# Optimization experiments

Hardware: AMD Instinct MI355X
Metric: run time of the kernel (lower is better)

Reference implementation:

```python
import jax, jax.numpy as jnp
import numpy as np
import math

INPUT_FRAMES = 12
FUTURE_FRAMES = 26
T_STEPS = INPUT_FRAMES + FUTURE_FRAMES - 1  # 37
HD = 64   # hidden_dim
D = 16    # d_attn
CIN = 3   # input channels (time='stable')
COUT = 2  # output_dim
H, W = 24, 48


def conv2d(x, w, b, pad):
    # x: (N,C,H,W), w: (O,I,kh,kw)
    y = jax.lax.conv_general_dilated(x, w, (1, 1), [(pad, pad), (pad, pad)],
                                     dimension_numbers=('NCHW', 'OIHW', 'NCHW'))
    return y + b[None, :, None, None]


def spatial_attn(q, k, v):
    # q,k,v: (N,C,S); attention over spatial dim S
    scale = 1.0 / math.sqrt(q.shape[1])
    scores = jnp.einsum('ncs,nct->nst', q, k) * scale  # (N,S,S)
    a = jax.nn.softmax(scores, axis=-1)
    return jnp.einsum('nst,nct->ncs', a, v)


def setup_inputs() -> dict:
    key = jax.random.key(0)
    ks = jax.random.split(key, 8)
    s = 0.05
    inp = {
        'input_x': jax.random.normal(ks[0], (16, T_STEPS, H, W, CIN), dtype=jnp.float32),
        # ConvLSTM gate conv: in = CIN+HD, out = 4*HD, 3x3
        'conv_w': jax.random.normal(ks[1], (4 * HD, CIN + HD, 3, 3), dtype=jnp.float32) * s,
        'conv_b': jnp.zeros((4 * HD,), jnp.float32),
        # SA memory module
        'h_w': jax.random.normal(ks[2], (3 * D, HD, 1, 1), dtype=jnp.float32) * s,
        'h_b': jnp.zeros((3 * D,), jnp.float32),
        'm_w': jax.random.normal(ks[3], (2 * D, HD, 1, 1), dtype=jnp.float32) * s,
        'm_b': jnp.zeros((2 * D,), jnp.float32),
        'z_w': jax.random.normal(ks[4], (D, 2 * D, 1, 1), dtype=jnp.float32) * s,
        'z_b': jnp.zeros((D,), jnp.float32),
        'o_w': jax.random.normal(ks[5], (3 * HD, HD + D, 3, 3), dtype=jnp.float32) * s,
        'o_b': jnp.zeros((3 * HD,), jnp.float32),
        # final 1x1 projection to output_dim
        'out_w': jax.random.normal(ks[6], (COUT, HD, 1, 1), dtype=jnp.float32) * s,
        'out_b': jnp.zeros((COUT,), jnp.float32),
    }
    return inp


def reference(input_x, conv_w, conv_b, h_w, h_b, m_w, m_b, z_w, z_b, o_w, o_b, out_w, out_b):
    x = jnp.transpose(input_x, (0, 1, 4, 2, 3))  # (N,T,C,H,W)
    N = x.shape[0]
    S = H * W

    h0 = jnp.zeros((N, HD, H, W), x.dtype)
    carry0 = (h0, h0, h0, jnp.zeros((N, COUT, H, W), x.dtype))

    def step(carry, inp_t):
        h, c, m, prev_out = carry
        xt, t = inp_t  # xt: (N,CIN,H,W), t: scalar
        autoreg = jnp.concatenate([prev_out, xt[:, 2:]], axis=1)
        feed = jnp.where(t < INPUT_FRAMES, xt, autoreg)
        # ConvLSTM gates
        comb = conv2d(jnp.concatenate([feed, h], axis=1), conv_w, conv_b, 1)
        ci, cf, co, cg = jnp.split(comb, 4, axis=1)
        i = jax.nn.sigmoid(ci)
        f = jax.nn.sigmoid(cf)
        o = jax.nn.sigmoid(co)
        g = jnp.tanh(cg)
        c = f * c + i * g
        h = o * jnp.tanh(c)
        # self-attention memory
        hq, hk, hv = jnp.split(conv2d(h, h_w, h_b, 0), 3, axis=1)
        mk, mv = jnp.split(conv2d(m, m_w, m_b, 0), 2, axis=1)
        Zh = spatial_attn(hq.reshape(N, D, S), hk.reshape(N, D, S), hv.reshape(N, D, S))
        Zm = spatial_attn(hq.reshape(N, D, S), mk.reshape(N, D, S), mv.reshape(N, D, S))
        Z = conv2d(jnp.concatenate([Zh.reshape(N, D, H, W), Zm.reshape(N, D, H, W)], axis=1), z_w, z_b, 0)
        iog = conv2d(jnp.concatenate([Z, h], axis=1), o_w, o_b, 1)
        si, sg, so = jnp.split(iog, 3, axis=1)
        si = jax.nn.sigmoid(si)
        sg = jnp.tanh(sg)
        m = si * sg + (1.0 - si) * m
        h = jax.nn.sigmoid(so) * m
        out = conv2d(h, out_w, out_b, 0)
        return (h, c, m, out), out

    xs = (jnp.transpose(x, (1, 0, 2, 3, 4)), jnp.arange(T_STEPS))
    _, outs = jax.lax.scan(step, carry0, xs)
    outputs = jnp.transpose(outs, (1, 0, 2, 3, 4))  # (N,T,COUT,H,W)

    nino = outputs[:, -FUTURE_FRAMES:, 0, 10:13, 19:30].mean(axis=(2, 3))  # (N,26)
    nino_pred = (nino[:, :-2] + nino[:, 1:-1] + nino[:, 2:]) / 3.0          # (N,24)
    return outputs, nino_pred
```

## Files before the change

kernel.cpp:

```cpp
#include <hip/hip_runtime.h>
#include <math.h>

#define HD 64
#define DATT 16
#define NCIN 3
#define NCOUT 2
#define HH 24
#define WW 48
#define SS (HH*WW)
#define NB 16
#define TSTEPS 37
#define INPUT_FRAMES 12

#define PR 26
#define PC 52
#define PHW (PR*PC)

#define OFF_H     0
#define OFF_C     1384448
#define OFF_M     2564096
#define OFF_FEED  3743744
#define OFF_Z     3808640
#define ZERO_END  4154752
#define OFF_QKV   4154752
#define OFF_MKV   5039488
#define OFF_HB    5629312
#define OFF_IOG   8873344
#define OFF_BF2   12412288
#define OFF_BF    12596864

typedef __attribute__((ext_vector_type(8))) short short8;
typedef __attribute__((ext_vector_type(4))) float f32x4;

__device__ __forceinline__ float sigmoidf_(float x) {
    return 1.0f / (1.0f + __expf(-x));
}
__device__ __forceinline__ unsigned short f2bf(float f) {
    unsigned u = __float_as_uint(f);
    unsigned r = (u + 0x7fffu + ((u >> 16) & 1u)) >> 16;
    return (unsigned short)r;
}
__device__ __forceinline__ float bf2f(unsigned short b) {
    return __uint_as_float(((unsigned)b) << 16);
}
__device__ __forceinline__ unsigned packbf(float f) {
    unsigned short hi = f2bf(f);
    unsigned short lo = f2bf(f - bf2f(hi));
    return ((unsigned)lo << 16) | (unsigned)hi;
}
__device__ __forceinline__ float unpackbf(unsigned pk) {
    return __uint_as_float(pk << 16) + __uint_as_float(pk & 0xffff0000u);
}
__device__ __forceinline__ unsigned cvt_pk_bf16(float a, float b) {
    unsigned r;
    asm("v_cvt_pk_bf16_f32 %0, %1, %2" : "=v"(r) : "v"(a), "v"(b));
    return r;
}
__device__ __forceinline__ int permrow(int t) {
    int kb = t >> 5, tl = t & 31;
    int quad = tl >> 3, rr = tl & 7;
    return kb * 32 + ((rr >= 4) ? 16 : 0) + quad * 4 + (rr & 3);
}

__global__ void k_zero(float* __restrict__ p, int n4) {
    int i = blockIdx.x * blockDim.x + threadIdx.x;
    if (i < n4) ((float4*)p)[i] = make_float4(0.f, 0.f, 0.f, 0.f);
}

__global__ void k_prep_bf2(const float* __restrict__ cw, unsigned short* __restrict__ bbuf) {
    int idx = blockIdx.x * 256 + threadIdx.x;
    if (idx >= 344064) return;
    int j    = idx & 7;
    int lane = (idx >> 3) & 63;
    int ki   = (idx >> 9) % 21;
    int nt   = (idx / 10752) % 16;
    int p    = idx / 172032;
    int k = ki * 32 + (lane >> 4) * 8 + j;
    int ncol = nt * 16 + (lane & 15);
    unsigned short v = 0;
    if (k < 648) {
        int c = k % 72, kt = k / 72;
        if (c < 67) {
            float w = cw[ncol * 603 + c * 9 + kt];
            unsigned short hi = f2bf(w);
            v = (p == 0) ? hi : f2bf(w - bf2f(hi));
        }
    }
    bbuf[idx] = v;
}

__global__ void k_prep_bf(const float* __restrict__ ow, unsigned short* __restrict__ bbuf) {
    int idx = blockIdx.x * 256 + threadIdx.x;
    if (idx >= 282624) return;
    int j    = idx & 7;
    int lane = (idx >> 3) & 63;
    int ki   = (idx >> 9) % 23;
    int nt   = (idx / 11776) % 12;
    int p    = idx / 141312;
    int k = ki * 32 + (lane >> 4) * 8 + j;
    int ncol = nt * 16 + (lane & 15);
    unsigned short v = 0;
    if (k < 720) {
        int c = k % 80, kt = k / 80;
        float w = ow[ncol * 720 + c * 9 + kt];
        unsigned short hi = f2bf(w);
        v = (p == 0) ? hi : f2bf(w - bf2f(hi));
    }
    bbuf[idx] = v;
}

__global__ void k_feed0(const float* __restrict__ x, unsigned* __restrict__ feed) {
    int i = blockIdx.x * blockDim.x + threadIdx.x;
    if (i >= NB * 3 * SS) return;
    int s = i % SS;
    int ch = (i / SS) % 3;
    int n = i / (3 * SS);
    int y = s / WW, xx = s % WW;
    float v = x[(((size_t)(n * TSTEPS + 0) * HH + y) * WW + xx) * NCIN + ch];
    feed[((size_t)(n * 3 + ch) * PR + (y + 1)) * PC + (xx + 1)] = packbf(v);
}

#define RSTR2 304
#define ZROW2 (156*RSTR2)
__global__ __launch_bounds__(256) void k_conv_lstm_mfma(
    const unsigned* __restrict__ feed, const unsigned* __restrict__ hin,
    const unsigned short* __restrict__ bbuf, const float* __restrict__ cb,
    float* __restrict__ c, unsigned* __restrict__ hout)
{
    __shared__ __align__(16) int lds[156 * 76 + 76 + 8];
    const int n  = blockIdx.x;
    const int nb = blockIdx.y;
    const int y0 = blockIdx.z;
    const int tid = threadIdx.x;

    const unsigned* fbase = feed + (size_t)n * 3 * PHW;
    const unsigned* hbase = hin + (size_t)n * HD * PHW;
    for (int e = tid; e < 1404; e += 256) {
        int grp = e / 156;
        int r2  = e - grp * 156;
        int pr = r2 / 52, pc = r2 - pr * 52;
        int cc0 = grp * 8;
        unsigned v[8];
#pragma unroll
        for (int j = 0; j < 8; ++j) {
            int cc = cc0 + j;
            unsigned t = 0;
            if (cc < 3)        t = fbase[(size_t)cc * PHW + (y0 + pr) * PC + pc];
            else if (cc < 67)  t = hbase[(size_t)(cc - 3) * PHW + (y0 + pr) * PC + pc];
            v[j] = t;
        }
        union { unsigned u[4]; short8 s; } hi8, lo8;
#pragma unroll
        for (int p = 0; p < 4; ++p) {
            hi8.u[p] = (v[2 * p] & 0xffffu) | (v[2 * p + 1] << 16);
            lo8.u[p] = (v[2 * p] >> 16) | (v[2 * p + 1] & 0xffff0000u);
        }
        char* rowp = (char*)lds + r2 * RSTR2 + cc0 * 2;
        *(short8*)rowp = hi8.s;
        *(short8*)(rowp + 144) = lo8.s;
    }
    for (int i = tid; i < 76; i += 256) lds[156 * 76 + i] = 0;
    __syncthreads();

    const int wv = tid >> 6;
    const int lane = tid & 63;
    const int mcol = lane & 15;
    const int quad = lane >> 4;

    f32x4 acc[2][3];
#pragma unroll
    for (int jg = 0; jg < 2; ++jg)
#pragma unroll
        for (int xt = 0; xt < 3; ++xt) acc[jg][xt] = (f32x4){0.f, 0.f, 0.f, 0.f};

    const unsigned short* b0 = bbuf + ((size_t)(wv * 4 + nb * 2 + 0) * 21) * 512 + lane * 8;
    const unsigned short* b1 = bbuf + ((size_t)(wv * 4 + nb * 2 + 1) * 21) * 512 + lane * 8;

    short8 cb0h = *(const short8*)(b0);
    short8 cb0l = *(const short8*)(b0 + 172032);
    short8 cb1h = *(const short8*)(b1);
    short8 cb1l = *(const short8*)(b1 + 172032);
    short8 pb0h = *(const short8*)(b0 + 512);
    short8 pb0l = *(const short8*)(b0 + 512 + 172032);
    short8 pb1h = *(const short8*)(b1 + 512);
    short8 pb1l = *(const short8*)(b1 + 512 + 172032);

    const char* lp = (const char*)lds;

    for (int ki = 0; ki < 21; ++ki) {
        int kn = (ki + 2 <= 20) ? (ki + 2) * 512 : 20 * 512;
        short8 qb0h = *(const short8*)(b0 + kn);
        short8 qb0l = *(const short8*)(b0 + kn + 172032);
        short8 qb1h = *(const short8*)(b1 + kn);
        short8 qb1l = *(const short8*)(b1 + kn + 172032);

        int k0 = ki * 32 + quad * 8;
        int abyte, stepb;
        if (k0 < 648) {
            int kt = k0 / 72;
            int c0 = k0 - kt * 72;
            int dy = kt / 3, dx = kt - dy * 3;
            abyte = (dy * 52 + mcol + dx) * RSTR2 + c0 * 2;
            stepb = 16 * RSTR2;
        } else {
            abyte = ZROW2; stepb = 0;
        }
        short8 xh0 = *(const short8*)(lp + abyte);
        short8 xl0 = *(const short8*)(lp + abyte + 144);
        short8 xh1 = *(const short8*)(lp + abyte + stepb);
        short8 xl1 = *(const short8*)(lp + abyte + stepb + 144);
        short8 xh2 = *(const short8*)(lp + abyte + 2 * stepb);
        short8 xl2 = *(const short8*)(lp + abyte + 2 * stepb + 144);

        acc[0][0] = __builtin_amdgcn_mfma_f32_16x16x32_bf16(xh0, cb0h, acc[0][0], 0, 0, 0);
        acc[0][0] = __builtin_amdgcn_mfma_f32_16x16x32_bf16(xh0, cb0l, acc[0][0], 0, 0, 0);
        acc[0][0] = __builtin_amdgcn_mfma_f32_16x16x32_bf16(xl0, cb0h, acc[0][0], 0, 0, 0);
        acc[1][0] = __builtin_amdgcn_mfma_f32_16x16x32_bf16(xh0, cb1h, acc[1][0], 0, 0, 0);
        acc[1][0] = __builtin_amdgcn_mfma_f32_16x16x32_bf16(xh0, cb1l, acc[1][0], 0, 0, 0);
        acc[1][0] = __builtin_amdgcn_mfma_f32_16x16x32_bf16(xl0, cb1h, acc[1][0], 0, 0, 0);
        acc[0][1] = __builtin_amdgcn_mfma_f32_16x16x32_bf16(xh1, cb0h, acc[0][1], 0, 0, 0);
        acc[0][1] = __builtin_amdgcn_mfma_f32_16x16x32_bf16(xh1, cb0l, acc[0][1], 0, 0, 0);
        acc[0][1] = __builtin_amdgcn_mfma_f32_16x16x32_bf16(xl1, cb0h, acc[0][1], 0, 0, 0);
        acc[1][1] = __builtin_amdgcn_mfma_f32_16x16x32_bf16(xh1, cb1h, acc[1][1], 0, 0, 0);
        acc[1][1] = __builtin_amdgcn_mfma_f32_16x16x32_bf16(xh1, cb1l, acc[1][1], 0, 0, 0);
        acc[1][1] = __builtin_amdgcn_mfma_f32_16x16x32_bf16(xl1, cb1h, acc[1][1], 0, 0, 0);
        acc[0][2] = __builtin_amdgcn_mfma_f32_16x16x32_bf16(xh2, cb0h, acc[0][2], 0, 0, 0);
        acc[0][2] = __builtin_amdgcn_mfma_f32_16x16x32_bf16(xh2, cb0l, acc[0][2], 0, 0, 0);
        acc[0][2] = __builtin_amdgcn_mfma_f32_16x16x32_bf16(xl2, cb0h, acc[0][2], 0, 0, 0);
        acc[1][2] = __builtin_amdgcn_mfma_f32_16x16x32_bf16(xh2, cb1h, acc[1][2], 0, 0, 0);
        acc[1][2] = __builtin_amdgcn_mfma_f32_16x16x32_bf16(xh2, cb1l, acc[1][2], 0, 0, 0);
        acc[1][2] = __builtin_amdgcn_mfma_f32_16x16x32_bf16(xl2, cb1h, acc[1][2], 0, 0, 0);

        cb0h = pb0h; cb0l = pb0l; cb1h = pb1h; cb1l = pb1l;
        pb0h = qb0h; pb0l = qb0l; pb1h = qb1h; pb1l = qb1l;
    }

    __syncthreads();
    float* exch = (float*)lds;
#pragma unroll
    for (int jg = 0; jg < 2; ++jg)
#pragma unroll
        for (int xt = 0; xt < 3; ++xt)
#pragma unroll
            for (int r = 0; r < 4; ++r)
                exch[((wv * 2 + jg) * 3 + xt) * 272 + (quad * 4 + r) * 17 + mcol] = acc[jg][xt][r];
    __syncthreads();

    const int ch32 = tid & 31;
    const int xg = tid >> 5;
    const int jg = ch32 >> 4, col = ch32 & 15;
    const int gch = nb * 32 + ch32;
    const float bi = cb[gch], bfv = cb[64 + gch], bo = cb[128 + gch], bg = cb[192 + gch];
    size_t cbase = ((size_t)(n * HD + gch) * HH + y0) * WW;
    unsigned* hp = hout + ((size_t)(n * HD + gch) * PR + y0 + 1) * PC + 1;
#pragma unroll
    for (int k = 0; k < 6; ++k) {
        int x = xg * 6 + k;
        int xt = x >> 4, row = x & 15;
        float iv = sigmoidf_(exch[((0 * 2 + jg) * 3 + xt) * 272 + row * 17 + col] + bi);
        float fv = sigmoidf_(exch[((1 * 2 + jg) * 3 + xt) * 272 + row * 17 + col] + bfv);
        float ov = sigmoidf_(exch[((2 * 2 + jg) * 3 + xt) * 272 + row * 17 + col] + bo);
        float gv = tanhf    (exch[((3 * 2 + jg) * 3 + xt) * 272 + row * 17 + col] + bg);
        float cold = c[cbase + x];
        float cn = fv * cold + iv * gv;
        float hn = ov * tanhf(cn);
        c[cbase + x] = cn;
        hp[x] = packbf(hn);
    }
}

#define RSTR 328
#define ZROW (156*RSTR)
__global__ __launch_bounds__(192) void k_conv_sa(
    const unsigned* __restrict__ Zin, const unsigned* __restrict__ hin,
    const unsigned short* __restrict__ bbuf, const float* __restrict__ ob,
    float* __restrict__ m, unsigned* __restrict__ hout)
{
    __shared__ __align__(16) int lds[156 * 82 + 82 + 8];
    const int n  = blockIdx.x;
    const int cbk = blockIdx.y;
    const int y0 = blockIdx.z;
    const int tid = threadIdx.x;

    const unsigned* zbase = Zin + (size_t)n * DATT * PHW;
    const unsigned* hbase = hin + (size_t)n * HD * PHW;
    for (int e = tid; e < 1560; e += 192) {
        int grp = e / 156;
        int r2  = e - grp * 156;
        int pr = r2 / 52, pc = r2 - pr * 52;
        int cc0 = grp * 8;
        unsigned v[8];
#pragma unroll
        for (int j = 0; j < 8; ++j) {
            int cc = cc0 + j;
            const unsigned* src = (cc < 16) ? (zbase + (size_t)cc * PHW)
                                            : (hbase + (size_t)(cc - 16) * PHW);
            v[j] = src[(y0 + pr) * PC + pc];
        }
        union { unsigned u[4]; short8 s; } hi8, lo8;
#pragma unroll
        for (int p = 0; p < 4; ++p) {
            hi8.u[p] = (v[2 * p] & 0xffffu) | (v[2 * p + 1] << 16);
            lo8.u[p] = (v[2 * p] >> 16) | (v[2 * p + 1] & 0xffff0000u);
        }
        char* rowp = (char*)lds + r2 * RSTR + cc0 * 2;
        *(short8*)rowp = hi8.s;
        *(short8*)(rowp + 160) = lo8.s;
    }
    for (int i = tid; i < 82; i += 192) lds[156 * 82 + i] = 0;
    __syncthreads();

    const int wv = tid >> 6;
    const int lane = tid & 63;
    const int mcol = lane & 15;
    const int quad = lane >> 4;

    f32x4 acc[2][3];
#pragma unroll
    for (int j = 0; j < 2; ++j)
#pragma unroll
        for (int xt = 0; xt < 3; ++xt) acc[j][xt] = (f32x4){0.f, 0.f, 0.f, 0.f};

    const unsigned short* b0 = bbuf + ((size_t)(wv * 4 + cbk * 2 + 0) * 23) * 512 + lane * 8;
    const unsigned short* b1 = bbuf + ((size_t)(wv * 4 + cbk * 2 + 1) * 23) * 512 + lane * 8;

    short8 cb0h = *(const short8*)(b0);
    short8 cb0l = *(const short8*)(b0 + 141312);
    short8 cb1h = *(const short8*)(b1);
    short8 cb1l = *(const short8*)(b1 + 141312);
    short8 pb0h = *(const short8*)(b0 + 512);
    short8 pb0l = *(const short8*)(b0 + 512 + 141312);
    short8 pb1h = *(const short8*)(b1 + 512);
    short8 pb1l = *(const short8*)(b1 + 512 + 141312);

    const char* lp = (const char*)lds;

    for (int ki = 0; ki < 23; ++ki) {
        int kn = (ki + 2 <= 22) ? (ki + 2) * 512 : 22 * 512;
        short8 qb0h = *(const short8*)(b0 + kn);
        short8 qb0l = *(const short8*)(b0 + kn + 141312);
        short8 qb1h = *(const short8*)(b1 + kn);
        short8 qb1l = *(const short8*)(b1 + kn + 141312);

        int k0 = ki * 32 + quad * 8;
        int abyte, stepb;
        if (k0 < 720) {
            int kt = k0 / 80;
            int c0 = k0 - kt * 80;
            int dy = kt / 3, dx = kt - dy * 3;
            abyte = (dy * 52 + mcol + dx) * RSTR + c0 * 2;
            stepb = 16 * RSTR;
        } else {
            abyte = ZROW; stepb = 0;
        }
        short8 xh0 = *(const short8*)(lp + abyte);
        short8 xl0 = *(const short8*)(lp + abyte + 160);
        short8 xh1 = *(const short8*)(lp + abyte + stepb);
        short8 xl1 = *(const short8*)(lp + abyte + stepb + 160);
        short8 xh2 = *(const short8*)(lp + abyte + 2 * stepb);
        short8 xl2 = *(const short8*)(lp + abyte + 2 * stepb + 160);

        acc[0][0] = __builtin_amdgcn_mfma_f32_16x16x32_bf16(xh0, cb0h, acc[0][0], 0, 0, 0);
        acc[0][0] = __builtin_amdgcn_mfma_f32_16x16x32_bf16(xh0, cb0l, acc[0][0], 0, 0, 0);
        acc[0][0] = __builtin_amdgcn_mfma_f32_16x16x32_bf16(xl0, cb0h, acc[0][0], 0, 0, 0);
        acc[1][0] = __builtin_amdgcn_mfma_f32_16x16x32_bf16(xh0, cb1h, acc[1][0], 0, 0, 0);
        acc[1][0] = __builtin_amdgcn_mfma_f32_16x16x32_bf16(xh0, cb1l, acc[1][0], 0, 0, 0);
        acc[1][0] = __builtin_amdgcn_mfma_f32_16x16x32_bf16(xl0, cb1h, acc[1][0], 0, 0, 0);
        acc[0][1] = __builtin_amdgcn_mfma_f32_16x16x32_bf16(xh1, cb0h, acc[0][1], 0, 0, 0);
        acc[0][1] = __builtin_amdgcn_mfma_f32_16x16x32_bf16(xh1, cb0l, acc[0][1], 0, 0, 0);
        acc[0][1] = __builtin_amdgcn_mfma_f32_16x16x32_bf16(xl1, cb0h, acc[0][1], 0, 0, 0);
        acc[1][1] = __builtin_amdgcn_mfma_f32_16x16x32_bf16(xh1, cb1h, acc[1][1], 0, 0, 0);
        acc[1][1] = __builtin_amdgcn_mfma_f32_16x16x32_bf16(xh1, cb1l, acc[1][1], 0, 0, 0);
        acc[1][1] = __builtin_amdgcn_mfma_f32_16x16x32_bf16(xl1, cb1h, acc[1][1], 0, 0, 0);
        acc[0][2] = __builtin_amdgcn_mfma_f32_16x16x32_bf16(xh2, cb0h, acc[0][2], 0, 0, 0);
        acc[0][2] = __builtin_amdgcn_mfma_f32_16x16x32_bf16(xh2, cb0l, acc[0][2], 0, 0, 0);
        acc[0][2] = __builtin_amdgcn_mfma_f32_16x16x32_bf16(xl2, cb0h, acc[0][2], 0, 0, 0);
        acc[1][2] = __builtin_amdgcn_mfma_f32_16x16x32_bf16(xh2, cb1h, acc[1][2], 0, 0, 0);
        acc[1][2] = __builtin_amdgcn_mfma_f32_16x16x32_bf16(xh2, cb1l, acc[1][2], 0, 0, 0);
        acc[1][2] = __builtin_amdgcn_mfma_f32_16x16x32_bf16(xl2, cb1h, acc[1][2], 0, 0, 0);

        cb0h = pb0h; cb0l = pb0l; cb1h = pb1h; cb1l = pb1l;
        pb0h = qb0h; pb0l = qb0l; pb1h = qb1h; pb1l = qb1l;
    }

    __syncthreads();
    float* exch = (float*)lds;
#pragma unroll
    for (int j = 0; j < 2; ++j)
#pragma unroll
        for (int xt = 0; xt < 3; ++xt)
#pragma unroll
            for (int r = 0; r < 4; ++r)
                exch[((wv * 2 + j) * 3 + xt) * 272 + (quad * 4 + r) * 17 + mcol] = acc[j][xt][r];
    __syncthreads();

    const int ch32 = tid & 31;
    const int xg = tid >> 5;
    const int jg = ch32 >> 4, col = ch32 & 15;
    const int gch = cbk * 32 + ch32;
    const float bsi = ob[gch], bsg = ob[64 + gch], bso = ob[128 + gch];
    float* mrow = m + ((size_t)(n * HD + gch) * HH + y0) * WW;
    unsigned* hp = hout + ((size_t)(n * HD + gch) * PR + y0 + 1) * PC + 1;
#pragma unroll
    for (int k = 0; k < 8; ++k) {
        int x = xg * 8 + k;
        int xt = x >> 4, row = x & 15;
        float si = sigmoidf_(exch[((0 * 2 + jg) * 3 + xt) * 272 + row * 17 + col] + bsi);
        float sg = tanhf    (exch[((1 * 2 + jg) * 3 + xt) * 272 + row * 17 + col] + bsg);
        float so =           exch[((2 * 2 + jg) * 3 + xt) * 272 + row * 17 + col] + bso;
        float mo = mrow[x];
        float mn = si * sg + (1.f - si) * mo;
        mrow[x] = mn;
        hp[x] = packbf(sigmoidf_(so) * mn);
    }
}

__global__ __launch_bounds__(256) void k_qkv(
    const unsigned* __restrict__ h, const float* __restrict__ m,
    const float* __restrict__ hw, const float* __restrict__ hb,
    const float* __restrict__ mw, const float* __restrict__ mb,
    unsigned short* __restrict__ pl) {
    __shared__ float lw[512];
    __shared__ float lb[8];
    const int g = blockIdx.y;
    const int tid = threadIdx.x;
    const float* wsrc = (g < 6) ? (hw + g * 512) : (mw + (g - 6) * 512);
    const float* bsrc = (g < 6) ? (hb + g * 8) : (mb + (g - 6) * 8);
    for (int i = tid; i < 512; i += 256) lw[i] = wsrc[i];
    if (tid < 8) lb[tid] = bsrc[tid];
    __syncthreads();

    int idx = blockIdx.x * 256 + tid;
    int s = idx % SS;
    int n = idx / SS;

    float reg[HD];
    if (g < 6) {
        int y = s / WW, x = s % WW;
        const unsigned* src = h + (size_t)n * HD * PHW + (y + 1) * PC + (x + 1);
#pragma unroll
        for (int ic = 0; ic < HD; ++ic) reg[ic] = unpackbf(src[ic * PHW]);
    } else {
        const float* src = m + (size_t)n * HD * SS + s;
#pragma unroll
        for (int ic = 0; ic < HD; ++ic) reg[ic] = src[ic * SS];
    }

    float out[8];
#pragma unroll
    for (int j = 0; j < 8; ++j) {
        const float* wr = &lw[j * HD];
        float a = lb[j];
#pragma unroll
        for (int ic = 0; ic < HD; ++ic) a += reg[ic] * wr[ic];
        out[j] = a;
    }

    unsigned short* bq  = pl;
    unsigned short* akh = pl + 294912;
    unsigned short* akm = pl + 589824;
    unsigned short* bvh = pl + 884736;
    unsigned short* bvm = pl + 1179648;
    const int c0 = (g & 1) * 8;

    if (g < 2) {
        unsigned w0 = (unsigned)f2bf(out[0]) | ((unsigned)f2bf(out[1]) << 16);
        unsigned w1 = (unsigned)f2bf(out[2]) | ((unsigned)f2bf(out[3]) << 16);
        unsigned w2 = (unsigned)f2bf(out[4]) | ((unsigned)f2bf(out[5]) << 16);
        unsigned w3 = (unsigned)f2bf(out[6]) | ((unsigned)f2bf(out[7]) << 16);
        *(uint4*)&bq[((size_t)n * SS + s) * 16 + c0] = make_uint4(w0, w1, w2, w3);
    } else if (g < 4 || (g >= 6 && g < 8)) {
        int row = permrow(s);
        unsigned short* base = (g < 4) ? akh : akm;
        unsigned w0 = (unsigned)f2bf(out[0]) | ((unsigned)f2bf(out[1]) << 16);
        unsigned w1 = (unsigned)f2bf(out[2]) | ((unsigned)f2bf(out[3]) << 16);
        unsigned w2 = (unsigned)f2bf(out[4]) | ((unsigned)f2bf(out[5]) << 16);
        unsigned w3 = (unsigned)f2bf(out[6]) | ((unsigned)f2bf(out[7]) << 16);
        *(uint4*)&base[((size_t)n * SS + row) * 16 + c0] = make_uint4(w0, w1, w2, w3);
    } else {
        unsigned short* base = (g < 6) ? bvh : bvm;
#pragma unroll
        for (int j = 0; j < 8; ++j)
            base[((size_t)n * 16 + c0 + j) * SS + s] = f2bf(out[j]);
    }
}

__global__ __launch_bounds__(256) void k_attn(
    const unsigned short* __restrict__ pl, const unsigned short* __restrict__ zbuf,
    const float* __restrict__ zw, const float* __restrict__ zb,
    unsigned* __restrict__ Z)
{
    __shared__ float ldsO[4][2][16][16];
    __shared__ float ldsF[2][16][16];
    __shared__ float ldsL[4][2][16];
    __shared__ float ldsLF[2][16];

    const int n   = blockIdx.x;
    const int qt  = blockIdx.y;
    const int tid = threadIdx.x;
    const int wv  = tid >> 6;
    const int lane = tid & 63;
    const int col  = lane & 15;
    const int quad = lane >> 4;
    const bool hi  = quad >= 2;

    const unsigned short* bq  = pl;
    const unsigned short* akh = pl + 294912;
    const unsigned short* akm = pl + 589824;
    const unsigned short* bvh = pl + 884736;
    const unsigned short* bvm = pl + 1179648;

    const size_t nb = (size_t)n * 18432;
    const int stepk = hi ? 0 : 512;
    const int subk  = hi ? 0 : 256;
    const unsigned short* qp  = hi ? zbuf : (bq  + nb + ((size_t)(qt * 16 + col)) * 16 + quad * 8);
    const unsigned short* khb = hi ? zbuf : (akh + nb + col * 16 + quad * 8);
    const unsigned short* kmb = hi ? zbuf : (akm + nb + col * 16 + quad * 8);
    const unsigned short* vhb = bvh + nb + (size_t)col * SS + quad * 8;
    const unsigned short* vmb = bvm + nb + (size_t)col * SS + quad * 8;

    short8 qf = *(const short8*)qp;

    f32x4 oh = (f32x4){0.f,0.f,0.f,0.f}, om = (f32x4){0.f,0.f,0.f,0.f};
    float lh = 0.f, lm = 0.f;
    const int kb0 = wv * 9, kb1 = kb0 + 9;
    for (int kb = kb0; kb < kb1; ++kb) {
        const unsigned short* kh0 = khb + (size_t)kb * stepk;
        const unsigned short* km0 = kmb + (size_t)kb * stepk;
        short8 khA = *(const short8*)kh0;
        short8 khB = *(const short8*)(kh0 + subk);
        short8 kmA = *(const short8*)km0;
        short8 kmB = *(const short8*)(km0 + subk);
        short8 vh  = *(const short8*)(vhb + (size_t)kb * 32);
        short8 vm  = *(const short8*)(vmb + (size_t)kb * 32);
        const f32x4 z4 = (f32x4){0.f,0.f,0.f,0.f};
        f32x4 sA = __builtin_amdgcn_mfma_f32_16x16x32_bf16(khA, qf, z4, 0, 0, 0);
        f32x4 sB = __builtin_amdgcn_mfma_f32_16x16x32_bf16(khB, qf, z4, 0, 0, 0);
        f32x4 tA = __builtin_amdgcn_mfma_f32_16x16x32_bf16(kmA, qf, z4, 0, 0, 0);
        f32x4 tB = __builtin_amdgcn_mfma_f32_16x16x32_bf16(kmB, qf, z4, 0, 0, 0);

        float pa0 = __expf(0.25f * sA[0]), pa1 = __expf(0.25f * sA[1]);
        float pa2 = __expf(0.25f * sA[2]), pa3 = __expf(0.25f * sA[3]);
        float pb0 = __expf(0.25f * sB[0]), pb1 = __expf(0.25f * sB[1]);
        float pb2 = __expf(0.25f * sB[2]), pb3 = __expf(0.25f * sB[3]);
        lh += (pa0 + pa1 + pa2 + pa3) + (pb0 + pb1 + pb2 + pb3);
        union { unsigned u[4]; short8 v; } ph;
        ph.u[0] = cvt_pk_bf16(pa0, pa1); ph.u[1] = cvt_pk_bf16(pa2, pa3);
        ph.u[2] = cvt_pk_bf16(pb0, pb1); ph.u[3] = cvt_pk_bf16(pb2, pb3);
        oh = __builtin_amdgcn_mfma_f32_16x16x32_bf16(ph.v, vh, oh, 0, 0, 0);

        float qa0 = __expf(0.25f * tA[0]), qa1 = __expf(0.25f * tA[1]);
        float qa2 = __expf(0.25f * tA[2]), qa3 = __expf(0.25f * tA[3]);
        float qb0 = __expf(0.25f * tB[0]), qb1 = __expf(0.25f * tB[1]);
        float qb2 = __expf(0.25f * tB[2]), qb3 = __expf(0.25f * tB[3]);
        lm += (qa0 + qa1 + qa2 + qa3) + (qb0 + qb1 + qb2 + qb3);
        union { unsigned u[4]; short8 v; } pm;
        pm.u[0] = cvt_pk_bf16(qa0, qa1); pm.u[1] = cvt_pk_bf16(qa2, qa3);
        pm.u[2] = cvt_pk_bf16(qb0, qb1); pm.u[3] = cvt_pk_bf16(qb2, qb3);
        om = __builtin_amdgcn_mfma_f32_16x16x32_bf16(pm.v, vm, om, 0, 0, 0);
    }

    lh += __shfl_xor(lh, 16); lh += __shfl_xor(lh, 32);
    lm += __shfl_xor(lm, 16); lm += __shfl_xor(lm, 32);

#pragma unroll
    for (int r = 0; r < 4; ++r) {
        ldsO[wv][0][quad * 4 + r][col] = oh[r];
        ldsO[wv][1][quad * 4 + r][col] = om[r];
    }
    if (lane < 16) { ldsL[wv][0][lane] = lh; ldsL[wv][1][lane] = lm; }
    __syncthreads();

    if (tid < 128) {
        int a_ = tid >> 6, rem = tid & 63, q_ = rem >> 2, j4 = (rem & 3) * 4;
        float4 s4 = make_float4(0.f, 0.f, 0.f, 0.f);
#pragma unroll
        for (int w = 0; w < 4; ++w) {
            float4 v = *(const float4*)&ldsO[w][a_][q_][j4];
            s4.x += v.x; s4.y += v.y; s4.z += v.z; s4.w += v.w;
        }
        *(float4*)&ldsF[a_][q_][j4] = s4;
    } else if (tid < 160) {
        int e = tid - 128, a_ = e >> 4, q_ = e & 15;
        ldsLF[a_][q_] = ldsL[0][a_][q_] + ldsL[1][a_][q_] +
                        ldsL[2][a_][q_] + ldsL[3][a_][q_];
    }
    __syncthreads();

    const int q  = tid & 15;
    const int zc = tid >> 4;
    float iLh = 1.f / ldsLF[0][q], iLm = 1.f / ldsLF[1][q];
    const float* zr = zw + zc * 32;
    float a = zb[zc];
#pragma unroll
    for (int j = 0; j < 16; ++j)
        a += zr[j] * (ldsF[0][q][j] * iLh) + zr[16 + j] * (ldsF[1][q][j] * iLm);
    int s = qt * 16 + q;
    int y = s / WW, x = s % WW;
    Z[((size_t)(n * DATT + zc) * PR + y + 1) * PC + x + 1] = packbf(a);
}

__global__ void k_out_feed(const unsigned* __restrict__ h, const float* __restrict__ ow,
                           const float* __restrict__ ob, const float* __restrict__ x,
                           float* __restrict__ outbuf, unsigned* __restrict__ feed, int t) {
    int idx = blockIdx.x * 256 + threadIdx.x;
    if (idx >= NB * SS) return;
    int s = idx % SS;
    int n = idx / SS;
    int y = s / WW, xx = s % WW;
    const unsigned* src = h + (size_t)n * HD * PHW + (y + 1) * PC + (xx + 1);
    float o0 = ob[0], o1 = ob[1];
#pragma unroll
    for (int ic = 0; ic < HD; ++ic) {
        float r = unpackbf(src[ic * PHW]);
        o0 += r * ow[ic];
        o1 += r * ow[HD + ic];
    }
    outbuf[(((size_t)n * TSTEPS + t) * NCOUT + 0) * SS + s] = o0;
    outbuf[(((size_t)n * TSTEPS + t) * NCOUT + 1) * SS + s] = o1;

    if (t + 1 < TSTEPS) {
        int t1 = t + 1;
        const float* xp = &x[(((size_t)(n * TSTEPS + t1) * HH + y) * WW + xx) * NCIN];
        float f0, f1, f2 = xp[2];
        if (t1 < INPUT_FRAMES) { f0 = xp[0]; f1 = xp[1]; }
        else { f0 = o0; f1 = o1; }
        size_t fb = ((size_t)(n * 3 + 0) * PR + y + 1) * PC + xx + 1;
        feed[fb] = packbf(f0);
        feed[fb + PHW] = packbf(f1);
        feed[fb + 2 * (size_t)PHW] = packbf(f2);
    }
}

__global__ void k_nino(const float* __restrict__ outbuf, float* __restrict__ pred) {
    int tidx = threadIdx.x;
    if (tidx >= 16 * 24) return;
    int j = tidx % 24;
    int n = tidx / 24;
    float acc = 0.f;
    for (int f = j; f < j + 3; ++f) {
        int t = 11 + f;
        const float* p = &outbuf[(((size_t)n * TSTEPS + t) * NCOUT + 0) * SS];
        float sloc = 0.f;
        for (int y = 10; y <= 12; ++y)
            for (int x = 19; x <= 29; ++x)
                sloc += p[y * WW + x];
        acc += sloc * (1.f / 33.f);
    }
    pred[n * 24 + j] = acc * (1.f / 3.f);
}

extern "C" void kernel_launch(void* const* d_in, const int* in_sizes, int n_in,
                              void* d_out, int out_size, void* d_ws, size_t ws_size,
                              hipStream_t stream) {
    const float* x      = (const float*)d_in[0];
    const float* conv_w = (const float*)d_in[1];
    const float* conv_b = (const float*)d_in[2];
    const float* h_w    = (const float*)d_in[3];
    const float* h_b    = (const float*)d_in[4];
    const float* m_w    = (const float*)d_in[5];
    const float* m_b    = (const float*)d_in[6];
    const float* z_w    = (const float*)d_in[7];
    const float* z_b    = (const float*)d_in[8];
    const float* o_w    = (const float*)d_in[9];
    const float* o_b    = (const float*)d_in[10];
    const float* out_w  = (const float*)d_in[11];
    const float* out_b  = (const float*)d_in[12];

    float* ws   = (float*)d_ws;
    unsigned* hA    = (unsigned*)(ws + OFF_H);
    float* c    = ws + OFF_C;
    float* m    = ws + OFF_M;
    unsigned* feedp = (unsigned*)(ws + OFF_FEED);
    unsigned* Zp    = (unsigned*)(ws + OFF_Z);
    unsigned* hB    = (unsigned*)(ws + OFF_HB);
    unsigned short* bf2 = (unsigned short*)(ws + OFF_BF2);
    unsigned short* bf  = (unsigned short*)(ws + OFF_BF);
    unsigned short* planes = (unsigned short*)(ws + OFF_QKV);
    const unsigned short* zbuf = (const unsigned short*)(ws + OFF_MKV);
    float* outp = (float*)d_out;

    k_zero<<<4058, 256, 0, stream>>>(ws, 1038688);
    k_zero<<<1352, 256, 0, stream>>>(ws + OFF_HB, 346112);
    k_zero<<<1, 64, 0, stream>>>(ws + OFF_MKV, 16);
    k_prep_bf2<<<1344, 256, 0, stream>>>(conv_w, bf2);
    k_prep_bf<<<1104, 256, 0, stream>>>(o_w, bf);
    k_feed0<<<216, 256, 0, stream>>>(x, feedp);

    for (int t = 0; t < TSTEPS; ++t) {
        k_conv_lstm_mfma<<<dim3(16, 2, 24), 256, 0, stream>>>(feedp, hB, bf2, conv_b, c, hA);
        k_qkv<<<dim3(72, 10), 256, 0, stream>>>(hA, m, h_w, h_b, m_w, m_b, planes);
        k_attn<<<dim3(16, 72), 256, 0, stream>>>(planes, zbuf, z_w, z_b, Zp);
        k_conv_sa<<<dim3(16, 2, 24), 192, 0, stream>>>(Zp, hA, bf, o_b, m, hB);
        k_out_feed<<<72, 256, 0, stream>>>(hB, out_w, out_b, x, outp, feedp, t);
    }
    k_nino<<<1, 384, 0, stream>>>(outp, outp + (size_t)NB * TSTEPS * NCOUT * SS);
}
```

Before: 4.205 ms.

## Merge channel-block halves into one workgroup for both MFMA conv kernels

Both 3x3 gate-conv kernels previously launched separate workgroups for each half of the output channels, so every workgroup staged the same input halo rows into LDS twice across the grid. The halves are now folded into one workgroup with double the waves (512 and 384 threads), so the halo is loaded and repacked once and shared by all output channels. This halves the grid size and the redundant global loads and LDS packing, but it also halves the number of workgroups (384 per launch), which may reduce occupancy and latency hiding on a large GPU.

```diff
diff --git a/kernel.cpp b/kernel.cpp
--- a/kernel.cpp
+++ b/kernel.cpp
@@ -122,20 +122,19 @@
 
 #define RSTR2 304
 #define ZROW2 (156*RSTR2)
-__global__ __launch_bounds__(256) void k_conv_lstm_mfma(
+__global__ __launch_bounds__(512) void k_conv_lstm_mfma(
     const unsigned* __restrict__ feed, const unsigned* __restrict__ hin,
     const unsigned short* __restrict__ bbuf, const float* __restrict__ cb,
     float* __restrict__ c, unsigned* __restrict__ hout)
 {
-    __shared__ __align__(16) int lds[156 * 76 + 76 + 8];
+    __shared__ __align__(16) int lds[13056];
     const int n  = blockIdx.x;
-    const int nb = blockIdx.y;
-    const int y0 = blockIdx.z;
+    const int y0 = blockIdx.y;
     const int tid = threadIdx.x;
 
     const unsigned* fbase = feed + (size_t)n * 3 * PHW;
     const unsigned* hbase = hin + (size_t)n * HD * PHW;
-    for (int e = tid; e < 1404; e += 256) {
+    for (int e = tid; e < 1404; e += 512) {
         int grp = e / 156;
         int r2  = e - grp * 156;
         int pr = r2 / 52, pc = r2 - pr * 52;
@@ -159,10 +158,12 @@
         *(short8*)rowp = hi8.s;
         *(short8*)(rowp + 144) = lo8.s;
     }
-    for (int i = tid; i < 76; i += 256) lds[156 * 76 + i] = 0;
+    if (tid < 76) lds[156 * 76 + tid] = 0;
     __syncthreads();
 
     const int wv = tid >> 6;
+    const int gate = wv & 3;
+    const int nbw  = wv >> 2;
     const int lane = tid & 63;
     const int mcol = lane & 15;
     const int quad = lane >> 4;
@@ -173,8 +174,8 @@
 #pragma unroll
         for (int xt = 0; xt < 3; ++xt) acc[jg][xt] = (f32x4){0.f, 0.f, 0.f, 0.f};
 
-    const unsigned short* b0 = bbuf + ((size_t)(wv * 4 + nb * 2 + 0) * 21) * 512 + lane * 8;
-    const unsigned short* b1 = bbuf + ((size_t)(wv * 4 + nb * 2 + 1) * 21) * 512 + lane * 8;
+    const unsigned short* b0 = bbuf + ((size_t)(gate * 4 + nbw * 2 + 0) * 21) * 512 + lane * 8;
+    const unsigned short* b1 = bbuf + ((size_t)(gate * 4 + nbw * 2 + 1) * 21) * 512 + lane * 8;
 
     short8 cb0h = *(const short8*)(b0);
     short8 cb0l = *(const short8*)(b0 + 172032);
@@ -243,24 +244,25 @@
         for (int xt = 0; xt < 3; ++xt)
 #pragma unroll
             for (int r = 0; r < 4; ++r)
-                exch[((wv * 2 + jg) * 3 + xt) * 272 + (quad * 4 + r) * 17 + mcol] = acc[jg][xt][r];
-    __syncthreads();
-
-    const int ch32 = tid & 31;
-    const int xg = tid >> 5;
-    const int jg = ch32 >> 4, col = ch32 & 15;
-    const int gch = nb * 32 + ch32;
-    const float bi = cb[gch], bfv = cb[64 + gch], bo = cb[128 + gch], bg = cb[192 + gch];
-    size_t cbase = ((size_t)(n * HD + gch) * HH + y0) * WW;
-    unsigned* hp = hout + ((size_t)(n * HD + gch) * PR + y0 + 1) * PC + 1;
+                exch[((gate * 4 + nbw * 2 + jg) * 3 + xt) * 272 + (quad * 4 + r) * 17 + mcol]
+                    = acc[jg][xt][r];
+    __syncthreads();
+
+    const int ch64 = tid & 63;
+    const int xg = tid >> 6;
+    const int enb = ch64 >> 5, ejg = (ch64 >> 4) & 1, col = ch64 & 15;
+    const int fb = enb * 2 + ejg;
+    const float bi = cb[ch64], bfv = cb[64 + ch64], bo = cb[128 + ch64], bg = cb[192 + ch64];
+    size_t cbase = ((size_t)(n * HD + ch64) * HH + y0) * WW;
+    unsigned* hp = hout + ((size_t)(n * HD + ch64) * PR + y0 + 1) * PC + 1;
 #pragma unroll
     for (int k = 0; k < 6; ++k) {
         int x = xg * 6 + k;
         int xt = x >> 4, row = x & 15;
-        float iv = sigmoidf_(exch[((0 * 2 + jg) * 3 + xt) * 272 + row * 17 + col] + bi);
-        float fv = sigmoidf_(exch[((1 * 2 + jg) * 3 + xt) * 272 + row * 17 + col] + bfv);
-        float ov = sigmoidf_(exch[((2 * 2 + jg) * 3 + xt) * 272 + row * 17 + col] + bo);
-        float gv = tanhf    (exch[((3 * 2 + jg) * 3 + xt) * 272 + row * 17 + col] + bg);
+        float iv = sigmoidf_(exch[((0 + fb) * 3 + xt) * 272 + row * 17 + col] + bi);
+        float fv = sigmoidf_(exch[((4 + fb) * 3 + xt) * 272 + row * 17 + col] + bfv);
+        float ov = sigmoidf_(exch[((8 + fb) * 3 + xt) * 272 + row * 17 + col] + bo);
+        float gv = tanhf    (exch[((12 + fb) * 3 + xt) * 272 + row * 17 + col] + bg);
         float cold = c[cbase + x];
         float cn = fv * cold + iv * gv;
         float hn = ov * tanhf(cn);
@@ -271,20 +273,19 @@
 
 #define RSTR 328
 #define ZROW (156*RSTR)
-__global__ __launch_bounds__(192) void k_conv_sa(
+__global__ __launch_bounds__(384) void k_conv_sa(
     const unsigned* __restrict__ Zin, const unsigned* __restrict__ hin,
     const unsigned short* __restrict__ bbuf, const float* __restrict__ ob,
     float* __restrict__ m, unsigned* __restrict__ hout)
 {
-    __shared__ __align__(16) int lds[156 * 82 + 82 + 8];
+    __shared__ __align__(16) int lds[12882];
     const int n  = blockIdx.x;
-    const int cbk = blockIdx.y;
-    const int y0 = blockIdx.z;
+    const int y0 = blockIdx.y;
     const int tid = threadIdx.x;
 
     const unsigned* zbase = Zin + (size_t)n * DATT * PHW;
     const unsigned* hbase = hin + (size_t)n * HD * PHW;
-    for (int e = tid; e < 1560; e += 192) {
+    for (int e = tid; e < 1560; e += 384) {
         int grp = e / 156;
         int r2  = e - grp * 156;
         int pr = r2 / 52, pc = r2 - pr * 52;
@@ -307,10 +308,12 @@
         *(short8*)rowp = hi8.s;
         *(short8*)(rowp + 160) = lo8.s;
     }
-    for (int i = tid; i < 82; i += 192) lds[156 * 82 + i] = 0;
+    if (tid < 82) lds[156 * 82 + tid] = 0;
     __syncthreads();
 
     const int wv = tid >> 6;
+    const int cbw = (wv >= 3) ? 1 : 0;
+    const int gate = wv - cbw * 3;
     const int lane = tid & 63;
     const int mcol = lane & 15;
     const int quad = lane >> 4;
@@ -321,8 +324,8 @@
 #pragma unroll
         for (int xt = 0; xt < 3; ++xt) acc[j][xt] = (f32x4){0.f, 0.f, 0.f, 0.f};
 
-    const unsigned short* b0 = bbuf + ((size_t)(wv * 4 + cbk * 2 + 0) * 23) * 512 + lane * 8;
-    const unsigned short* b1 = bbuf + ((size_t)(wv * 4 + cbk * 2 + 1) * 23) * 512 + lane * 8;
+    const unsigned short* b0 = bbuf + ((size_t)(gate * 4 + cbw * 2 + 0) * 23) * 512 + lane * 8;
+    const unsigned short* b1 = bbuf + ((size_t)(gate * 4 + cbw * 2 + 1) * 23) * 512 + lane * 8;
 
     short8 cb0h = *(const short8*)(b0);
     short8 cb0l = *(const short8*)(b0 + 141312);
@@ -391,23 +394,23 @@
         for (int xt = 0; xt < 3; ++xt)
 #pragma unroll
             for (int r = 0; r < 4; ++r)
-                exch[((wv * 2 + j) * 3 + xt) * 272 + (quad * 4 + r) * 17 + mcol] = acc[j][xt][r];
-    __syncthreads();
-
-    const int ch32 = tid & 31;
-    const int xg = tid >> 5;
-    const int jg = ch32 >> 4, col = ch32 & 15;
-    const int gch = cbk * 32 + ch32;
-    const float bsi = ob[gch], bsg = ob[64 + gch], bso = ob[128 + gch];
-    float* mrow = m + ((size_t)(n * HD + gch) * HH + y0) * WW;
-    unsigned* hp = hout + ((size_t)(n * HD + gch) * PR + y0 + 1) * PC + 1;
+                exch[(((cbw * 3 + gate) * 2 + j) * 3 + xt) * 272 + (quad * 4 + r) * 17 + mcol]
+                    = acc[j][xt][r];
+    __syncthreads();
+
+    const int ch64 = tid & 63;
+    const int xg = tid >> 6;
+    const int ecb = ch64 >> 5, ejg = (ch64 >> 4) & 1, col = ch64 & 15;
+    const float bsi = ob[ch64], bsg = ob[64 + ch64], bso = ob[128 + ch64];
+    float* mrow = m + ((size_t)(n * HD + ch64) * HH + y0) * WW;
+    unsigned* hp = hout + ((size_t)(n * HD + ch64) * PR + y0 + 1) * PC + 1;
 #pragma unroll
     for (int k = 0; k < 8; ++k) {
         int x = xg * 8 + k;
         int xt = x >> 4, row = x & 15;
-        float si = sigmoidf_(exch[((0 * 2 + jg) * 3 + xt) * 272 + row * 17 + col] + bsi);
-        float sg = tanhf    (exch[((1 * 2 + jg) * 3 + xt) * 272 + row * 17 + col] + bsg);
-        float so =           exch[((2 * 2 + jg) * 3 + xt) * 272 + row * 17 + col] + bso;
+        float si = sigmoidf_(exch[(((ecb * 3 + 0) * 2 + ejg) * 3 + xt) * 272 + row * 17 + col] + bsi);
+        float sg = tanhf    (exch[(((ecb * 3 + 1) * 2 + ejg) * 3 + xt) * 272 + row * 17 + col] + bsg);
+        float so =           exch[(((ecb * 3 + 2) * 2 + ejg) * 3 + xt) * 272 + row * 17 + col] + bso;
         float mo = mrow[x];
         float mn = si * sg + (1.f - si) * mo;
         mrow[x] = mn;
@@ -688,10 +691,10 @@
     k_feed0<<<216, 256, 0, stream>>>(x, feedp);
 
     for (int t = 0; t < TSTEPS; ++t) {
-        k_conv_lstm_mfma<<<dim3(16, 2, 24), 256, 0, stream>>>(feedp, hB, bf2, conv_b, c, hA);
+        k_conv_lstm_mfma<<<dim3(16, 24), 512, 0, stream>>>(feedp, hB, bf2, conv_b, c, hA);
         k_qkv<<<dim3(72, 10), 256, 0, stream>>>(hA, m, h_w, h_b, m_w, m_b, planes);
         k_attn<<<dim3(16, 72), 256, 0, stream>>>(planes, zbuf, z_w, z_b, Zp);
-        k_conv_sa<<<dim3(16, 2, 24), 192, 0, stream>>>(Zp, hA, bf, o_b, m, hB);
+        k_conv_sa<<<dim3(16, 24), 384, 0, stream>>>(Zp, hA, bf, o_b, m, hB);
         k_out_feed<<<72, 256, 0, stream>>>(hB, out_w, out_b, x, outp, feedp, t);
     }
     k_nino<<<1, 384, 0, stream>>>(outp, outp + (size_t)NB * TSTEPS * NCOUT * SS);
```

Result: slower. 5.054 ms (+20.2%).
